# Performance work log

Measured on AMD Instinct MI355X. Metric: run time of the kernel, lower is better.

Reference implementation:

```python
import jax, jax.numpy as jnp
import numpy as np

T, B = 4096, 8192


def setup_inputs() -> dict:
    key = jax.random.key(0)
    k1, k2 = jax.random.split(key)
    # binary Bernoulli(0.5) observations, shape [T, B, 1]
    inputs = jnp.round(jax.random.uniform(k1, (T, B, 1), dtype=jnp.float32))
    # decay_rate = exp(-1 / 10**loglifetime), loglifetime ~ U(0.5, 2.5)
    loglifetime = jax.random.uniform(k2, (), minval=0.5, maxval=2.5)
    decay_rate = jnp.exp(-1.0 / (10.0 ** loglifetime)).astype(jnp.float32)
    return {"inputs": inputs, "decay_rate": decay_rate}


def _forward(inputs, decay_rate):
    # order == 1 ('transition' estimate): bigram leaky counts
    x = inputs[:, :, 0]                      # [T, B]
    n_seqs = x.shape[1]
    z = jnp.zeros((n_seqs,), dtype=inputs.dtype)
    d = decay_rate

    def step(carry, x_t):
        n10, n11, na0, na1, prev = carry
        n10 = d * (n10 + x_t * (1.0 - prev))   # ones after a 0
        n11 = d * (n11 + x_t * prev)           # ones after a 1
        na0 = d * (na0 + (1.0 - prev))         # all after a 0
        na1 = d * (na1 + prev)                 # all after a 1
        return (n10, n11, na0, na1, x_t), (n10, n11, na0, na1)

    _, (n10s, n11s, na0s, na1s) = jax.lax.scan(step, (z, z, z, z, z), x)

    N_ONES_PRIOR, N_ALL_PRIOR = 1.0, 2.0
    p0 = (n10s + N_ONES_PRIOR) / (na0s + N_ALL_PRIOR)   # [T, B]
    p1 = (n11s + N_ONES_PRIOR) / (na1s + N_ALL_PRIOR)   # [T, B]
    # prediction conditioned on current observation
    pred = p0 * (1.0 - x) + p1 * x                      # [T, B]
    return pred[:, :, None]                             # [T, B, 1]


def reference(inputs, decay_rate):
    return _forward(inputs, decay_rate)
```

## Files before the change

kernel.cpp:

```cpp
#include <hip/hip_runtime.h>


constexpr int T_DIM  = 4096;
constexpr int B_DIM  = 8192;
constexpr int NCHUNK = 64;
constexpr int CLEN   = T_DIM / NCHUNK;
constexpr int VEC    = 2;
constexpr int UNROLL = 8;


__global__ __launch_bounds__(256) void partial_kernel(
    const float* __restrict__ x, const float* __restrict__ dptr,
    float* __restrict__ ws)
{
    const float d  = *dptr;
    const int   c  = blockIdx.y;
    const int   b0 = (blockIdx.x * blockDim.x + threadIdx.x) * VEC;
    const long  t0 = (long)c * CLEN;

    float prev[VEC];
    if (c == 0) {
        prev[0] = prev[1] = 0.0f;
    } else {
        const float2 pv = *reinterpret_cast<const float2*>(x + (t0 - 1) * B_DIM + b0);
        prev[0] = pv.x; prev[1] = pv.y;
    }

    float n10[VEC] = {0,0}, n11[VEC] = {0,0}, na0[VEC] = {0,0}, na1[VEC] = {0,0};

    const float* p = x + t0 * B_DIM + b0;
    for (int kk = 0; kk < CLEN; kk += UNROLL) {
        float2 xv[UNROLL];
        #pragma unroll
        for (int u = 0; u < UNROLL; ++u)
            xv[u] = *reinterpret_cast<const float2*>(p + (size_t)u * B_DIM);
        p += (size_t)UNROLL * B_DIM;
        #pragma unroll
        for (int u = 0; u < UNROLL; ++u) {
            const float xs[VEC] = {xv[u].x, xv[u].y};
            #pragma unroll
            for (int j = 0; j < VEC; ++j) {
                const float xt = xs[j];
                const float pr = prev[j];
                const float om = 1.0f - pr;
                n10[j] = d * (n10[j] + xt * om);
                n11[j] = d * (n11[j] + xt * pr);
                na0[j] = d * (na0[j] + om);
                na1[j] = d * (na1[j] + pr);
                prev[j] = xt;
            }
        }
    }

    float* w = ws + (size_t)c * B_DIM + b0;
    *reinterpret_cast<float2*>(w + (size_t)0 * NCHUNK * B_DIM) = make_float2(n10[0], n10[1]);
    *reinterpret_cast<float2*>(w + (size_t)1 * NCHUNK * B_DIM) = make_float2(n11[0], n11[1]);
    *reinterpret_cast<float2*>(w + (size_t)2 * NCHUNK * B_DIM) = make_float2(na0[0], na0[1]);
    *reinterpret_cast<float2*>(w + (size_t)3 * NCHUNK * B_DIM) = make_float2(na1[0], na1[1]);
}

__global__ __launch_bounds__(256) void scan_kernel(
    const float* __restrict__ dptr, float* __restrict__ ws)
{
    float dL = *dptr;
    #pragma unroll
    for (int i = 0; i < 6; ++i) dL = dL * dL;

    const int tid = blockIdx.x * blockDim.x + threadIdx.x;
    float* p = ws + (size_t)(tid / B_DIM) * NCHUNK * B_DIM + (tid % B_DIM);

    float s = 0.f;
    for (int c = 0; c < NCHUNK; ++c) {
        const float l = p[(size_t)c * B_DIM];
        p[(size_t)c * B_DIM] = s;
        s = dL * s + l;
    }
}

__global__ __launch_bounds__(256) void final_kernel(
    const float* __restrict__ x, const float* __restrict__ dptr,
    const float* __restrict__ ws, float* __restrict__ out)
{
    const float d  = *dptr;
    const int   c  = blockIdx.y;
    const int   b0 = (blockIdx.x * blockDim.x + threadIdx.x) * VEC;
    const long  t0 = (long)c * CLEN;

    float prev[VEC];
    if (c == 0) {
        prev[0] = prev[1] = 0.0f;
    } else {
        const float2 pv = *reinterpret_cast<const float2*>(x + (t0 - 1) * B_DIM + b0);
        prev[0] = pv.x; prev[1] = pv.y;
    }

    const float* w = ws + (size_t)c * B_DIM + b0;
    const float2 s0 = *reinterpret_cast<const float2*>(w + (size_t)0 * NCHUNK * B_DIM);
    const float2 s1 = *reinterpret_cast<const float2*>(w + (size_t)1 * NCHUNK * B_DIM);
    const float2 s2 = *reinterpret_cast<const float2*>(w + (size_t)2 * NCHUNK * B_DIM);
    const float2 s3 = *reinterpret_cast<const float2*>(w + (size_t)3 * NCHUNK * B_DIM);
    float n10[VEC] = {s0.x, s0.y};
    float n11[VEC] = {s1.x, s1.y};
    float na0[VEC] = {s2.x, s2.y};
    float na1[VEC] = {s3.x, s3.y};

    const float* p = x   + t0 * B_DIM + b0;
    float*       q = out + t0 * B_DIM + b0;
    for (int kk = 0; kk < CLEN; kk += UNROLL) {
        float2 xv[UNROLL];
        #pragma unroll
        for (int u = 0; u < UNROLL; ++u)
            xv[u] = *reinterpret_cast<const float2*>(p + (size_t)u * B_DIM);
        p += (size_t)UNROLL * B_DIM;
        #pragma unroll
        for (int u = 0; u < UNROLL; ++u) {
            const float xs[VEC] = {xv[u].x, xv[u].y};
            float pr2[VEC];
            #pragma unroll
            for (int j = 0; j < VEC; ++j) {
                const float xt = xs[j];
                const float pv = prev[j];
                const float om = 1.0f - pv;
                n10[j] = d * (n10[j] + xt * om);
                n11[j] = d * (n11[j] + xt * pv);
                na0[j] = d * (na0[j] + om);
                na1[j] = d * (na1[j] + pv);
                prev[j] = xt;
                const float p0 = (n10[j] + 1.0f) * __builtin_amdgcn_rcpf(na0[j] + 2.0f);
                const float p1 = (n11[j] + 1.0f) * __builtin_amdgcn_rcpf(na1[j] + 2.0f);
                pr2[j] = p0 + (p1 - p0) * xt;
            }
            *reinterpret_cast<float2*>(q + (size_t)u * B_DIM) = make_float2(pr2[0], pr2[1]);
        }
        q += (size_t)UNROLL * B_DIM;
    }
}

extern "C" void kernel_launch(void* const* d_in, const int* in_sizes, int n_in,
                              void* d_out, int out_size, void* d_ws, size_t ws_size,
                              hipStream_t stream) {
    const float* x  = (const float*)d_in[0];
    const float* dr = (const float*)d_in[1];
    float* ws  = (float*)d_ws;
    float* out = (float*)d_out;

    dim3 blk(256);
    dim3 grid1(B_DIM / VEC / 256, NCHUNK);
    partial_kernel<<<grid1, blk, 0, stream>>>(x, dr, ws);
    scan_kernel<<<(4 * B_DIM) / 256, blk, 0, stream>>>(dr, ws);
    final_kernel<<<grid1, blk, 0, stream>>>(x, dr, ws, out);
}
```

Before: 264.7 us.

## Fuse cross-chunk carry scan into final kernel and use nontemporal output stores

Removes the separate scan kernel launch. Each final-kernel thread now recomputes its own chunk's starting state by folding all preceding chunk partials with the chunk-length decay power. This drops one launch and the scan's serial read-modify-write pass over the workspace. The cost is redundant work: later chunks re-read up to 63 partials each, quadratic in chunk count but cache-friendly. Output stores are switched to nontemporal to reduce cache pollution from the streaming writes.

```diff
diff --git a/kernel.cpp b/kernel.cpp
--- a/kernel.cpp
+++ b/kernel.cpp
@@ -7,6 +7,8 @@
 constexpr int CLEN   = T_DIM / NCHUNK;
 constexpr int VEC    = 2;
 constexpr int UNROLL = 8;
+
+typedef float v2f __attribute__((ext_vector_type(2)));
 
 
 __global__ __launch_bounds__(256) void partial_kernel(
@@ -59,32 +61,37 @@
     *reinterpret_cast<float2*>(w + (size_t)3 * NCHUNK * B_DIM) = make_float2(na1[0], na1[1]);
 }
 
-__global__ __launch_bounds__(256) void scan_kernel(
-    const float* __restrict__ dptr, float* __restrict__ ws)
-{
-    float dL = *dptr;
-    #pragma unroll
-    for (int i = 0; i < 6; ++i) dL = dL * dL;
-
-    const int tid = blockIdx.x * blockDim.x + threadIdx.x;
-    float* p = ws + (size_t)(tid / B_DIM) * NCHUNK * B_DIM + (tid % B_DIM);
-
-    float s = 0.f;
-    for (int c = 0; c < NCHUNK; ++c) {
-        const float l = p[(size_t)c * B_DIM];
-        p[(size_t)c * B_DIM] = s;
-        s = dL * s + l;
-    }
-}
-
 __global__ __launch_bounds__(256) void final_kernel(
     const float* __restrict__ x, const float* __restrict__ dptr,
     const float* __restrict__ ws, float* __restrict__ out)
 {
     const float d  = *dptr;
+    float dL = d;
+    #pragma unroll
+    for (int i = 0; i < 6; ++i) dL = dL * dL;
+
     const int   c  = blockIdx.y;
     const int   b0 = (blockIdx.x * blockDim.x + threadIdx.x) * VEC;
     const long  t0 = (long)c * CLEN;
+
+    float n10[VEC] = {0,0}, n11[VEC] = {0,0}, na0[VEC] = {0,0}, na1[VEC] = {0,0};
+    {
+        const float* w0 = ws + (size_t)0 * NCHUNK * B_DIM + b0;
+        const float* w1 = ws + (size_t)1 * NCHUNK * B_DIM + b0;
+        const float* w2 = ws + (size_t)2 * NCHUNK * B_DIM + b0;
+        const float* w3 = ws + (size_t)3 * NCHUNK * B_DIM + b0;
+        #pragma unroll 4
+        for (int j = 0; j < c; ++j) {
+            const float2 l0 = *reinterpret_cast<const float2*>(w0 + (size_t)j * B_DIM);
+            const float2 l1 = *reinterpret_cast<const float2*>(w1 + (size_t)j * B_DIM);
+            const float2 l2 = *reinterpret_cast<const float2*>(w2 + (size_t)j * B_DIM);
+            const float2 l3 = *reinterpret_cast<const float2*>(w3 + (size_t)j * B_DIM);
+            n10[0] = dL * n10[0] + l0.x;  n10[1] = dL * n10[1] + l0.y;
+            n11[0] = dL * n11[0] + l1.x;  n11[1] = dL * n11[1] + l1.y;
+            na0[0] = dL * na0[0] + l2.x;  na0[1] = dL * na0[1] + l2.y;
+            na1[0] = dL * na1[0] + l3.x;  na1[1] = dL * na1[1] + l3.y;
+        }
+    }
 
     float prev[VEC];
     if (c == 0) {
@@ -93,16 +100,6 @@
         const float2 pv = *reinterpret_cast<const float2*>(x + (t0 - 1) * B_DIM + b0);
         prev[0] = pv.x; prev[1] = pv.y;
     }
-
-    const float* w = ws + (size_t)c * B_DIM + b0;
-    const float2 s0 = *reinterpret_cast<const float2*>(w + (size_t)0 * NCHUNK * B_DIM);
-    const float2 s1 = *reinterpret_cast<const float2*>(w + (size_t)1 * NCHUNK * B_DIM);
-    const float2 s2 = *reinterpret_cast<const float2*>(w + (size_t)2 * NCHUNK * B_DIM);
-    const float2 s3 = *reinterpret_cast<const float2*>(w + (size_t)3 * NCHUNK * B_DIM);
-    float n10[VEC] = {s0.x, s0.y};
-    float n11[VEC] = {s1.x, s1.y};
-    float na0[VEC] = {s2.x, s2.y};
-    float na1[VEC] = {s3.x, s3.y};
 
     const float* p = x   + t0 * B_DIM + b0;
     float*       q = out + t0 * B_DIM + b0;
@@ -130,7 +127,8 @@
                 const float p1 = (n11[j] + 1.0f) * __builtin_amdgcn_rcpf(na1[j] + 2.0f);
                 pr2[j] = p0 + (p1 - p0) * xt;
             }
-            *reinterpret_cast<float2*>(q + (size_t)u * B_DIM) = make_float2(pr2[0], pr2[1]);
+            v2f ov; ov.x = pr2[0]; ov.y = pr2[1];
+            __builtin_nontemporal_store(ov, reinterpret_cast<v2f*>(q + (size_t)u * B_DIM));
         }
         q += (size_t)UNROLL * B_DIM;
     }
@@ -147,6 +145,5 @@
     dim3 blk(256);
     dim3 grid1(B_DIM / VEC / 256, NCHUNK);
     partial_kernel<<<grid1, blk, 0, stream>>>(x, dr, ws);
-    scan_kernel<<<(4 * B_DIM) / 256, blk, 0, stream>>>(dr, ws);
     final_kernel<<<grid1, blk, 0, stream>>>(x, dr, ws, out);
 }
```

Measured after the change: 256.6 us. 1.03x faster.

## Bit-pack binary inputs in partial pass so final pass skips rereading x

Applied to the files above, without the earlier changes.

The partial kernel now packs each chunk's 64 binary observations per sequence into a 64-bit mask and stores it in the workspace. The final kernel rebuilds x_t and the previous value from these masks instead of rereading the 128MB input, which removes roughly a third of the total DRAM traffic. It also preloads all scan values into registers in the scan kernel and uses nontemporal stores for the output. The packing relies on the inputs being exactly 0 or 1, which the task defines, and it adds a small extra workspace write.

```diff
diff --git a/kernel.cpp b/kernel.cpp
--- a/kernel.cpp
+++ b/kernel.cpp
@@ -7,6 +7,9 @@
 constexpr int CLEN   = T_DIM / NCHUNK;
 constexpr int VEC    = 2;
 constexpr int UNROLL = 8;
+
+typedef float v2f __attribute__((ext_vector_type(2)));
+typedef unsigned long long u64;
 
 
 __global__ __launch_bounds__(256) void partial_kernel(
@@ -27,6 +30,7 @@
     }
 
     float n10[VEC] = {0,0}, n11[VEC] = {0,0}, na0[VEC] = {0,0}, na1[VEC] = {0,0};
+    u64 mask[VEC] = {0ull, 0ull};
 
     const float* p = x + t0 * B_DIM + b0;
     for (int kk = 0; kk < CLEN; kk += UNROLL) {
@@ -37,10 +41,12 @@
         p += (size_t)UNROLL * B_DIM;
         #pragma unroll
         for (int u = 0; u < UNROLL; ++u) {
+            const int   k = kk + u;
             const float xs[VEC] = {xv[u].x, xv[u].y};
             #pragma unroll
             for (int j = 0; j < VEC; ++j) {
                 const float xt = xs[j];
+                mask[j] |= (u64)(unsigned)xt << k;
                 const float pr = prev[j];
                 const float om = 1.0f - pr;
                 n10[j] = d * (n10[j] + xt * om);
@@ -57,6 +63,10 @@
     *reinterpret_cast<float2*>(w + (size_t)1 * NCHUNK * B_DIM) = make_float2(n11[0], n11[1]);
     *reinterpret_cast<float2*>(w + (size_t)2 * NCHUNK * B_DIM) = make_float2(na0[0], na0[1]);
     *reinterpret_cast<float2*>(w + (size_t)3 * NCHUNK * B_DIM) = make_float2(na1[0], na1[1]);
+
+    u64* bits = reinterpret_cast<u64*>(ws + (size_t)4 * NCHUNK * B_DIM);
+    bits[(size_t)c * B_DIM + b0]     = mask[0];
+    bits[(size_t)c * B_DIM + b0 + 1] = mask[1];
 }
 
 __global__ __launch_bounds__(256) void scan_kernel(
@@ -67,32 +77,27 @@
     for (int i = 0; i < 6; ++i) dL = dL * dL;
 
     const int tid = blockIdx.x * blockDim.x + threadIdx.x;
-    float* p = ws + (size_t)(tid / B_DIM) * NCHUNK * B_DIM + (tid % B_DIM);
+    float* p = ws + (size_t)(tid >> 13) * NCHUNK * B_DIM + (tid & (B_DIM - 1));
+
+    float l[NCHUNK];
+    #pragma unroll
+    for (int c = 0; c < NCHUNK; ++c) l[c] = p[(size_t)c * B_DIM];
 
     float s = 0.f;
+    #pragma unroll
     for (int c = 0; c < NCHUNK; ++c) {
-        const float l = p[(size_t)c * B_DIM];
         p[(size_t)c * B_DIM] = s;
-        s = dL * s + l;
+        s = dL * s + l[c];
     }
 }
 
 __global__ __launch_bounds__(256) void final_kernel(
-    const float* __restrict__ x, const float* __restrict__ dptr,
-    const float* __restrict__ ws, float* __restrict__ out)
+    const float* __restrict__ dptr, const float* __restrict__ ws,
+    float* __restrict__ out)
 {
     const float d  = *dptr;
     const int   c  = blockIdx.y;
     const int   b0 = (blockIdx.x * blockDim.x + threadIdx.x) * VEC;
-    const long  t0 = (long)c * CLEN;
-
-    float prev[VEC];
-    if (c == 0) {
-        prev[0] = prev[1] = 0.0f;
-    } else {
-        const float2 pv = *reinterpret_cast<const float2*>(x + (t0 - 1) * B_DIM + b0);
-        prev[0] = pv.x; prev[1] = pv.y;
-    }
 
     const float* w = ws + (size_t)c * B_DIM + b0;
     const float2 s0 = *reinterpret_cast<const float2*>(w + (size_t)0 * NCHUNK * B_DIM);
@@ -104,21 +109,30 @@
     float na0[VEC] = {s2.x, s2.y};
     float na1[VEC] = {s3.x, s3.y};
 
-    const float* p = x   + t0 * B_DIM + b0;
-    float*       q = out + t0 * B_DIM + b0;
+    const u64* bits = reinterpret_cast<const u64*>(ws + (size_t)4 * NCHUNK * B_DIM);
+    u64 mask[VEC];
+    mask[0] = bits[(size_t)c * B_DIM + b0];
+    mask[1] = bits[(size_t)c * B_DIM + b0 + 1];
+
+    float prev[VEC];
+    if (c == 0) {
+        prev[0] = prev[1] = 0.0f;
+    } else {
+        const u64 pm0 = bits[(size_t)(c - 1) * B_DIM + b0];
+        const u64 pm1 = bits[(size_t)(c - 1) * B_DIM + b0 + 1];
+        prev[0] = (float)(unsigned)(pm0 >> 63);
+        prev[1] = (float)(unsigned)(pm1 >> 63);
+    }
+
+    float* q = out + (size_t)c * CLEN * B_DIM + b0;
     for (int kk = 0; kk < CLEN; kk += UNROLL) {
-        float2 xv[UNROLL];
-        #pragma unroll
-        for (int u = 0; u < UNROLL; ++u)
-            xv[u] = *reinterpret_cast<const float2*>(p + (size_t)u * B_DIM);
-        p += (size_t)UNROLL * B_DIM;
         #pragma unroll
         for (int u = 0; u < UNROLL; ++u) {
-            const float xs[VEC] = {xv[u].x, xv[u].y};
+            const int k = kk + u;
             float pr2[VEC];
             #pragma unroll
             for (int j = 0; j < VEC; ++j) {
-                const float xt = xs[j];
+                const float xt = (float)(unsigned)((mask[j] >> k) & 1ull);
                 const float pv = prev[j];
                 const float om = 1.0f - pv;
                 n10[j] = d * (n10[j] + xt * om);
@@ -130,7 +144,8 @@
                 const float p1 = (n11[j] + 1.0f) * __builtin_amdgcn_rcpf(na1[j] + 2.0f);
                 pr2[j] = p0 + (p1 - p0) * xt;
             }
-            *reinterpret_cast<float2*>(q + (size_t)u * B_DIM) = make_float2(pr2[0], pr2[1]);
+            v2f ov; ov.x = pr2[0]; ov.y = pr2[1];
+            __builtin_nontemporal_store(ov, reinterpret_cast<v2f*>(q + (size_t)u * B_DIM));
         }
         q += (size_t)UNROLL * B_DIM;
     }
@@ -148,5 +163,5 @@
     dim3 grid1(B_DIM / VEC / 256, NCHUNK);
     partial_kernel<<<grid1, blk, 0, stream>>>(x, dr, ws);
     scan_kernel<<<(4 * B_DIM) / 256, blk, 0, stream>>>(dr, ws);
-    final_kernel<<<grid1, blk, 0, stream>>>(x, dr, ws, out);
+    final_kernel<<<grid1, blk, 0, stream>>>(dr, ws, out);
 }
```

New measurement: 240.1 us. 1.1x faster.
